# Kernel tuning notes

Measured on AMD Instinct MI355X. Metric: run time of the kernel, lower is better.

## Reference

```python
import jax, jax.numpy as jnp
import numpy as np

DIM, NH, NKV = 1024, 16, 4
HD = DIM // NH  # 64
B, T = 2, 2048


def _rotary_freqs(seq_len, dim):
    inv_freq = 1.0 / (10000.0 ** (jnp.arange(0, dim, 2, dtype=jnp.float32) / dim))
    pos = jnp.arange(seq_len, dtype=jnp.float32)
    return pos[:, None] * inv_freq[None, :]  # [T, dim/2]


def _apply_rotary(x, freqs):
    # x: [B, H, T, HD]; freqs: [T, HD/2]
    x1, x2 = x[..., ::2], x[..., 1::2]
    cos, sin = jnp.cos(freqs), jnp.sin(freqs)
    # NOTE: faithful to source, second half is x1*sin - x2*cos (not +)
    return jnp.concatenate([x1 * cos - x2 * sin, x1 * sin - x2 * cos], axis=-1)


def setup_inputs() -> dict:
    key = jax.random.key(0)
    ks = jax.random.split(key, 5)
    s = 0.02
    return {
        "x": jax.random.normal(ks[0], (B, T, DIM), dtype=jnp.float32),
        "Wq": jax.random.normal(ks[1], (DIM, DIM), dtype=jnp.float32) * s,
        "bq": jnp.zeros((DIM,), jnp.float32),
        "Wk": jax.random.normal(ks[2], (DIM, NKV * HD), dtype=jnp.float32) * s,
        "bk": jnp.zeros((NKV * HD,), jnp.float32),
        "Wv": jax.random.normal(ks[3], (DIM, NKV * HD), dtype=jnp.float32) * s,
        "bv": jnp.zeros((NKV * HD,), jnp.float32),
        "Wo": jax.random.normal(ks[4], (DIM, DIM), dtype=jnp.float32) * s,
        "bo": jnp.zeros((DIM,), jnp.float32),
    }


def reference(x, Wq, bq, Wk, bk, Wv, bv, Wo, bo):
    Bx, Tx, C = x.shape
    q = (x @ Wq + bq).reshape(Bx, Tx, NH, HD).transpose(0, 2, 1, 3)   # [B,NH,T,HD]
    k = (x @ Wk + bk).reshape(Bx, Tx, NKV, HD).transpose(0, 2, 1, 3)  # [B,NKV,T,HD]
    v = (x @ Wv + bv).reshape(Bx, Tx, NKV, HD).transpose(0, 2, 1, 3)

    freqs = _rotary_freqs(Tx, HD)
    q = _apply_rotary(q, freqs)
    k = _apply_rotary(k, freqs)

    rep = NH // NKV
    k = jnp.repeat(k, rep, axis=1)  # [B,NH,T,HD]
    v = jnpp = jnp.repeat(v, rep, axis=1)

    scores = jnp.einsum('bhqd,bhkd->bhqk', q, k) / jnp.sqrt(jnp.float32(HD))
    causal = jnp.tril(jnp.ones((Tx, Tx), dtype=bool))
    scores = jnp.where(causal[None, None], scores, -jnp.inf)
    attn = jax.nn.softmax(scores, axis=-1)
    ctx = jnp.einsum('bhqk,bhkd->bhqd', attn, v)
    out = ctx.transpose(0, 2, 1, 3).reshape(Bx, Tx, C)
    return out @ Wo + bo
```

## Files before the change

### kernel.cpp

```cpp
#include <hip/hip_runtime.h>
#include <math.h>

#define DIM 1024
#define NH 16
#define NKV 4
#define HD 64
#define HALF 32
#define NB 2
#define SEQ 2048
#define KVD 256
#define MTOT 4096
#define QSCALE 0.18033688f
#define MBIAS 8.0f

typedef __bf16 bf16x8 __attribute__((ext_vector_type(8)));
typedef float f32x4 __attribute__((ext_vector_type(4)));
typedef unsigned short u16x8 __attribute__((ext_vector_type(8)));

#define MFMA16(a, b, c) __builtin_amdgcn_mfma_f32_16x16x32_bf16(a, b, c, 0, 0, 0)

__device__ __forceinline__ unsigned short f2bf(float f) {
    unsigned int u = __float_as_uint(f);
    u = (u + 0x7fffu + ((u >> 16) & 1u)) >> 16;
    return (unsigned short)u;
}

__device__ __forceinline__ unsigned cvt_pk(float lo, float hi) {
    unsigned r;
    asm("v_cvt_pk_bf16_f32 %0, %1, %2" : "=v"(r) : "v"(lo), "v"(hi));
    return r;
}

__device__ __forceinline__ void gll16(const unsigned short* g, unsigned short* l) {
    __builtin_amdgcn_global_load_lds((const __attribute__((address_space(1))) void*)g,
                                     (__attribute__((address_space(3))) void*)l, 16, 0, 0);
}

__global__ __launch_bounds__(256) void prep_kernel(
    const float* __restrict__ x,
    const float* __restrict__ Wq, const float* __restrict__ Wk,
    const float* __restrict__ Wv, const float* __restrict__ Wo,
    unsigned short* __restrict__ xb,
    unsigned short* __restrict__ qt, unsigned short* __restrict__ kt,
    unsigned short* __restrict__ vt, unsigned short* __restrict__ ot,
    float* __restrict__ cosb, float* __restrict__ sinb)
{
    __shared__ float tile[64][65];
    const int bx = blockIdx.x;
    const int tid = threadIdx.x;
    if (bx < 256) {
        int idx = bx * 256 + tid;
        int t = idx >> 5, d = idx & 31;
        float e = (float)(2 * d) / (float)HD;
        float invf = 1.0f / powf(10000.0f, e);
        float f = (float)t * invf;
        cosb[idx] = cosf(f);
        sinb[idx] = sinf(f);
    } else if (bx < 2304) {
        int i = ((bx - 256) * 256 + tid) * 8;
        float4 v0 = *(const float4*)&x[i];
        float4 v1 = *(const float4*)&x[i + 4];
        u16x8 o;
        o[0] = f2bf(v0.x); o[1] = f2bf(v0.y); o[2] = f2bf(v0.z); o[3] = f2bf(v0.w);
        o[4] = f2bf(v1.x); o[5] = f2bf(v1.y); o[6] = f2bf(v1.z); o[7] = f2bf(v1.w);
        *(u16x8*)&xb[i] = o;
    } else {
        int idx2 = bx - 2304;
        int z = idx2 >> 8, rem = idx2 & 255, xx = rem & 15, yy = rem >> 4;
        const float* W; unsigned short* Wt; int N;
        switch (z) {
            case 0: W = Wq; Wt = qt; N = DIM; break;
            case 1: W = Wk; Wt = kt; N = KVD; break;
            case 2: W = Wv; Wt = vt; N = KVD; break;
            default: W = Wo; Wt = ot; N = DIM; break;
        }
        const int n0 = xx * 64;
        if (n0 >= N) return;
        const int k0 = yy * 64;
        const int row = tid >> 2, coff = (tid & 3) * 16;
#pragma unroll
        for (int i = 0; i < 4; i++) {
            float4 v = *(const float4*)&W[(size_t)(k0 + row) * N + n0 + coff + i * 4];
            tile[row][coff + i * 4 + 0] = v.x; tile[row][coff + i * 4 + 1] = v.y;
            tile[row][coff + i * 4 + 2] = v.z; tile[row][coff + i * 4 + 3] = v.w;
        }
        __syncthreads();
        u16x8 a, b;
#pragma unroll
        for (int i = 0; i < 8; i++) a[i] = f2bf(tile[coff + i][row]);
#pragma unroll
        for (int i = 0; i < 8; i++) b[i] = f2bf(tile[coff + 8 + i][row]);
        *(u16x8*)&Wt[(size_t)(n0 + row) * DIM + k0 + coff] = a;
        *(u16x8*)&Wt[(size_t)(n0 + row) * DIM + k0 + coff + 8] = b;
    }
}

__global__ __launch_bounds__(256) void qkv_gemm_kernel(
    const unsigned short* __restrict__ xb,
    const unsigned short* __restrict__ wqt, const unsigned short* __restrict__ wkt,
    const unsigned short* __restrict__ wvt,
    const float* __restrict__ bq, const float* __restrict__ bk, const float* __restrict__ bv,
    const float* __restrict__ cosb, const float* __restrict__ sinb,
    unsigned short* __restrict__ qbuf, unsigned short* __restrict__ kbuf,
    unsigned short* __restrict__ vT)
{
    __shared__ unsigned short As[128 * 32];
    __shared__ unsigned short Bs[128 * 32];
    const int tid = threadIdx.x;
    const int lane = tid & 63, w = tid >> 6;
    const int l15 = lane & 15, lg = lane >> 4;
    const int bid = blockIdx.x;
    const int lid = (bid & 7) * 48 + (bid >> 3);
    const int m0 = (lid / 12) * 128;
    const int n0g = (lid % 12) * 128;

    const unsigned short* Wt; const float* bias; int n0, mode;
    if (n0g < DIM)            { Wt = wqt; bias = bq; n0 = n0g; mode = 0; }
    else if (n0g < DIM + KVD) { Wt = wkt; bias = bk; n0 = n0g - DIM; mode = 1; }
    else                      { Wt = wvt; bias = bv; n0 = n0g - DIM - KVD; mode = 2; }

    const int wr = w >> 1, wc = w & 1;

    f32x4 acc[4][4];
#pragma unroll
    for (int i = 0; i < 4; i++)
#pragma unroll
        for (int j = 0; j < 4; j++) acc[i][j] = (f32x4){0.f, 0.f, 0.f, 0.f};

    for (int k0 = 0; k0 < DIM; k0 += 32) {
        __syncthreads();
#pragma unroll
        for (int i = 0; i < 2; i++) {
            int S = i * 256 + w * 64 + lane;
            int r = S >> 2, c8 = (S & 3) * 8;
            gll16(xb + (size_t)(m0 + r) * DIM + k0 + c8, &As[(i * 256 + w * 64) * 8]);
            gll16(Wt + (size_t)(n0 + r) * DIM + k0 + c8, &Bs[(i * 256 + w * 64) * 8]);
        }
        __syncthreads();
        bf16x8 af[4], bfr[4];
#pragma unroll
        for (int r = 0; r < 4; r++)
            af[r] = *(const bf16x8*)&As[(wr * 64 + r * 16 + l15) * 32 + lg * 8];
#pragma unroll
        for (int c = 0; c < 4; c++)
            bfr[c] = *(const bf16x8*)&Bs[(wc * 64 + c * 16 + l15) * 32 + lg * 8];
#pragma unroll
        for (int r = 0; r < 4; r++)
#pragma unroll
            for (int c = 0; c < 4; c++)
                acc[r][c] = MFMA16(af[r], bfr[c], acc[r][c]);
    }

    const int nloc = n0 + wc * 64;
    const bool even = (l15 & 1) == 0;
#pragma unroll
    for (int rt = 0; rt < 4; rt++) {
#pragma unroll
        for (int ct = 0; ct < 4; ct++) {
            const int c = ct * 16 + l15;
            const float bsv = bias[nloc + c];
            if (mode == 2) {
                const int col = nloc + c;
                const int khh = col >> 6, d = col & 63;
                const int bb = m0 >> 11;
                const int t = (m0 & (SEQ - 1)) + wr * 64 + rt * 16 + lg * 4;
                float v0 = acc[rt][ct][0] + bsv;
                float v1 = acc[rt][ct][1] + bsv;
                float v2 = acc[rt][ct][2] + bsv;
                float v3 = acc[rt][ct][3] + bsv;
                unsigned short* dst = vT + ((size_t)(bb * NKV + khh) * 64 + d) * SEQ + t;
                *(uint2*)dst = make_uint2(cvt_pk(v0, v1), cvt_pk(v2, v3));
            } else {
                const int p = c >> 1;
#pragma unroll
                for (int q = 0; q < 4; q++) {
                    const int mrow = m0 + wr * 64 + rt * 16 + lg * 4 + q;
                    float val = acc[rt][ct][q] + bsv;
                    float prt = __shfl_xor(val, 1);
                    const int t = mrow & (SEQ - 1);
                    float cs = cosb[t * HALF + p];
                    float sn = sinb[t * HALF + p];
                    float outv = even ? (val * cs - prt * sn) : (prt * sn - val * cs);
                    int outc = even ? p : (p + 32);
                    if (mode == 0) qbuf[(size_t)mrow * DIM + nloc + outc] = f2bf(outv * QSCALE);
                    else           kbuf[(size_t)mrow * KVD + nloc + outc] = f2bf(outv);
                }
            }
        }
    }
}

__global__ __launch_bounds__(256) void attn_mfma_kernel(
    const unsigned short* __restrict__ qb, const unsigned short* __restrict__ kb,
    const unsigned short* __restrict__ vT, unsigned short* __restrict__ ctx)
{
    __shared__ unsigned short Qs[64 * 64];
    __shared__ unsigned short Ks[2][64 * 64];
    __shared__ unsigned short Vt[2][64 * 64];
    __shared__ unsigned Pw[4][16 * 32];

    const int tid = threadIdx.x;
    const int lane = tid & 63, w = tid >> 6;
    const int l15 = lane & 15, lg = lane >> 4;
    const int xpair = blockIdx.x;
    const int h = blockIdx.y;
    const int b = blockIdx.z;
    const int kh = h >> 2;

    const unsigned short* qg = qb + (size_t)b * SEQ * DIM + (size_t)h * HD;
    const unsigned short* kg = kb + (size_t)b * SEQ * KVD + (size_t)kh * HD;
    const unsigned short* vg = vT + ((size_t)(b * NKV + kh) * HD) * SEQ;

    const int qg_row = w * 16 + l15;
    const int swzd = (l15 & 7) << 3;
    unsigned* PW = &Pw[w][l15 * 32];
    const int pswz = (l15 & 7) << 2;

    const int S1 = w * 64 + lane, r1 = S1 >> 3, d81 = ((S1 & 7) ^ (r1 & 7)) * 8;
    const int S2 = 256 + w * 64 + lane, r2 = S2 >> 3, d82 = ((S2 & 7) ^ (r2 & 7)) * 8;

#pragma unroll 1
    for (int p = 0; p < 2; p++) {
        const int xt = (p == 0) ? xpair : (31 - xpair);
        const int q0 = xt * 64;

        gll16(qg + (size_t)(q0 + r1) * DIM + d81, &Qs[(w * 64) * 8]);
        gll16(qg + (size_t)(q0 + r2) * DIM + d82, &Qs[(256 + w * 64) * 8]);
        gll16(kg + (size_t)r1 * KVD + d81, &Ks[0][(w * 64) * 8]);
        gll16(vg + (size_t)r1 * SEQ + d81, &Vt[0][(w * 64) * 8]);
        gll16(kg + (size_t)r2 * KVD + d82, &Ks[0][(256 + w * 64) * 8]);
        gll16(vg + (size_t)r2 * SEQ + d82, &Vt[0][(256 + w * 64) * 8]);
        __syncthreads();

        bf16x8 bq0 = *(const bf16x8*)&Qs[qg_row * 64 + ((lg * 8) ^ swzd)];
        bf16x8 bq1 = *(const bf16x8*)&Qs[qg_row * 64 + ((32 + lg * 8) ^ swzd)];

        f32x4 o[4];
#pragma unroll
        for (int i = 0; i < 4; i++) o[i] = (f32x4){0.f, 0.f, 0.f, 0.f};
        float lrun = 0.f;

        const int nch = xt + 1;
#pragma unroll 1
        for (int ch = 0; ch < nch; ch++) {
            const int cur = ch & 1;
            if (ch + 1 < nch) {
                const int kv1 = (ch + 1) * 64;
                gll16(kg + (size_t)(kv1 + r1) * KVD + d81, &Ks[cur ^ 1][(w * 64) * 8]);
                gll16(vg + (size_t)r1 * SEQ + kv1 + d81,   &Vt[cur ^ 1][(w * 64) * 8]);
                gll16(kg + (size_t)(kv1 + r2) * KVD + d82, &Ks[cur ^ 1][(256 + w * 64) * 8]);
                gll16(vg + (size_t)r2 * SEQ + kv1 + d82,   &Vt[cur ^ 1][(256 + w * 64) * 8]);
            }

            f32x4 sacc[4];
#pragma unroll
            for (int i = 0; i < 4; i++) sacc[i] = (f32x4){0.f, 0.f, 0.f, 0.f};
            __builtin_amdgcn_s_setprio(1);
#pragma unroll
            for (int ct = 0; ct < 4; ct++) {
                const int kr = ct * 16 + l15;
                bf16x8 ak = *(const bf16x8*)&Ks[cur][kr * 64 + ((lg * 8) ^ swzd)];
                sacc[ct] = MFMA16(ak, bq0, sacc[ct]);
            }
#pragma unroll
            for (int ct = 0; ct < 4; ct++) {
                const int kr = ct * 16 + l15;
                bf16x8 ak = *(const bf16x8*)&Ks[cur][kr * 64 + ((32 + lg * 8) ^ swzd)];
                sacc[ct] = MFMA16(ak, bq1, sacc[ct]);
            }
            __builtin_amdgcn_s_setprio(0);

            const int kv0 = ch * 64;
            if (kv0 == q0) {
#pragma unroll
                for (int ct = 0; ct < 4; ct++)
#pragma unroll
                    for (int r = 0; r < 4; r++)
                        if (ct * 16 + lg * 4 + r > qg_row) sacc[ct][r] = -INFINITY;
            }

            float rs = 0.f;
            unsigned pk0[4], pk1[4];
#pragma unroll
            for (int ct = 0; ct < 4; ct++) {
                float p0 = exp2f(sacc[ct][0] - MBIAS);
                float p1 = exp2f(sacc[ct][1] - MBIAS);
                float p2 = exp2f(sacc[ct][2] - MBIAS);
                float p3 = exp2f(sacc[ct][3] - MBIAS);
                rs += (p0 + p1) + (p2 + p3);
                pk0[ct] = cvt_pk(p0, p1);
                pk1[ct] = cvt_pk(p2, p3);
            }
            rs += __shfl_xor(rs, 16);
            rs += __shfl_xor(rs, 32);
            lrun += rs;

#pragma unroll
            for (int ct = 0; ct < 4; ct++) {
                int wrd = (ct * 8 + lg * 2) ^ pswz;
                *(uint2*)&PW[wrd] = make_uint2(pk0[ct], pk1[ct]);
            }

            __builtin_amdgcn_s_setprio(1);
#pragma unroll
            for (int s = 0; s < 2; s++) {
                int wrd = (s * 16 + lg * 4) ^ pswz;
                bf16x8 ap = *(const bf16x8*)&PW[wrd];
#pragma unroll
                for (int dt = 0; dt < 4; dt++) {
                    const int d = dt * 16 + l15;
                    bf16x8 bv2 = *(const bf16x8*)&Vt[cur][d * 64 + ((s * 32 + lg * 8) ^ ((d & 7) << 3))];
                    o[dt] = MFMA16(ap, bv2, o[dt]);
                }
            }
            __builtin_amdgcn_s_setprio(0);

            __syncthreads();
        }

        float linv = 1.0f / lrun;
        float lb0 = __shfl(linv, lg * 4 + 0);
        float lb1 = __shfl(linv, lg * 4 + 1);
        float lb2 = __shfl(linv, lg * 4 + 2);
        float lb3 = __shfl(linv, lg * 4 + 3);
#pragma unroll
        for (int dt = 0; dt < 4; dt++) {
            const size_t base = (size_t)(b * SEQ + q0 + lg * 4) * DIM + h * HD + dt * 16 + l15;
            ctx[base + (size_t)(w * 16) * DIM]           = f2bf(o[dt][0] * lb0);
            ctx[base + (size_t)(w * 16 + 1) * DIM]       = f2bf(o[dt][1] * lb1);
            ctx[base + (size_t)(w * 16 + 2) * DIM]       = f2bf(o[dt][2] * lb2);
            ctx[base + (size_t)(w * 16 + 3) * DIM]       = f2bf(o[dt][3] * lb3);
        }
    }
}

__global__ __launch_bounds__(256) void outproj_kernel(
    const unsigned short* __restrict__ ctx, const unsigned short* __restrict__ wot,
    const float* __restrict__ bo, float* __restrict__ out)
{
    __shared__ unsigned short As[128 * 32];
    __shared__ unsigned short Bs[128 * 32];
    const int tid = threadIdx.x;
    const int lane = tid & 63, w = tid >> 6;
    const int l15 = lane & 15, lg = lane >> 4;
    const int bid = blockIdx.x;
    const int lid = (bid & 7) * 32 + (bid >> 3);
    const int m0 = (lid >> 3) * 128;
    const int n0 = (lid & 7) * 128;
    const int wr = w >> 1, wc = w & 1;

    f32x4 acc[4][4];
#pragma unroll
    for (int i = 0; i < 4; i++)
#pragma unroll
        for (int j = 0; j < 4; j++) acc[i][j] = (f32x4){0.f, 0.f, 0.f, 0.f};

    for (int k0 = 0; k0 < DIM; k0 += 32) {
        __syncthreads();
#pragma unroll
        for (int i = 0; i < 2; i++) {
            int S = i * 256 + w * 64 + lane;
            int r = S >> 2, c8 = (S & 3) * 8;
            gll16(ctx + (size_t)(m0 + r) * DIM + k0 + c8, &As[(i * 256 + w * 64) * 8]);
            gll16(wot + (size_t)(n0 + r) * DIM + k0 + c8, &Bs[(i * 256 + w * 64) * 8]);
        }
        __syncthreads();
        bf16x8 af[4], bfr[4];
#pragma unroll
        for (int r = 0; r < 4; r++)
            af[r] = *(const bf16x8*)&As[(wr * 64 + r * 16 + l15) * 32 + lg * 8];
#pragma unroll
        for (int c = 0; c < 4; c++)
            bfr[c] = *(const bf16x8*)&Bs[(wc * 64 + c * 16 + l15) * 32 + lg * 8];
#pragma unroll
        for (int r = 0; r < 4; r++)
#pragma unroll
            for (int c = 0; c < 4; c++)
                acc[r][c] = MFMA16(af[r], bfr[c], acc[r][c]);
    }

#pragma unroll
    for (int rt = 0; rt < 4; rt++) {
#pragma unroll
        for (int ct = 0; ct < 4; ct++) {
            const int ncol = n0 + wc * 64 + ct * 16 + l15;
            const float bsv = bo[ncol];
#pragma unroll
            for (int q = 0; q < 4; q++) {
                const int mrow = m0 + wr * 64 + rt * 16 + lg * 4 + q;
                out[(size_t)mrow * DIM + ncol] = acc[rt][ct][q] + bsv;
            }
        }
    }
}

extern "C" void kernel_launch(void* const* d_in, const int* in_sizes, int n_in,
                              void* d_out, int out_size, void* d_ws, size_t ws_size,
                              hipStream_t stream) {
    (void)in_sizes; (void)n_in; (void)out_size; (void)ws_size;
    const float* x  = (const float*)d_in[0];
    const float* Wq = (const float*)d_in[1];
    const float* bq = (const float*)d_in[2];
    const float* Wk = (const float*)d_in[3];
    const float* bk = (const float*)d_in[4];
    const float* Wv = (const float*)d_in[5];
    const float* bv = (const float*)d_in[6];
    const float* Wo = (const float*)d_in[7];
    const float* bo = (const float*)d_in[8];
    float* out = (float*)d_out;
    char* ws = (char*)d_ws;

    unsigned short* xb  = (unsigned short*)(ws);
    unsigned short* qbf = (unsigned short*)(ws + 8388608);
    unsigned short* kbf = (unsigned short*)(ws + 16777216);
    unsigned short* ctx = (unsigned short*)(ws + 20971520);
    unsigned short* wqt = (unsigned short*)(ws + 29360128);
    unsigned short* wkt = (unsigned short*)(ws + 31457280);
    unsigned short* wvt = (unsigned short*)(ws + 31981568);
    unsigned short* wot = (unsigned short*)(ws + 32505856);
    float* cosb = (float*)(ws + 34603008);
    float* sinb = (float*)(ws + 34865152);
    unsigned short* vTb = (unsigned short*)(ws + 35127296);

    hipLaunchKernelGGL(prep_kernel, dim3(3328), dim3(256), 0, stream,
                       x, Wq, Wk, Wv, Wo, xb, wqt, wkt, wvt, wot, cosb, sinb);
    hipLaunchKernelGGL(qkv_gemm_kernel, dim3(384), dim3(256), 0, stream,
                       xb, wqt, wkt, wvt, bq, bk, bv, cosb, sinb, qbf, kbf, vTb);
    hipLaunchKernelGGL(attn_mfma_kernel, dim3(16, NH, NB), dim3(256), 0, stream,
                       qbf, kbf, vTb, ctx);
    hipLaunchKernelGGL(outproj_kernel, dim3(256), dim3(256), 0, stream,
                       ctx, wot, bo, out);
}
```

Baseline: 112.4 us.

## Split paired query tiles into separate blocks and load Q directly to registers

The attention kernel now launches one block per 64-row query tile (32 tiles per head) instead of pairing a short and a long causal tile in one block. Tile order is rotated by the head/batch index to spread the long and short tiles across the grid. Q is read straight from global memory into registers, which drops the Q shared-memory buffer, and the row-sum shuffles are moved out of the inner loop to run once at the end. It also adds an occupancy hint of 4 blocks per CU. The cost is losing the built-in load balancing of paired tiles, so the grid now contains blocks with very uneven amounts of work.

```diff
diff --git a/kernel.cpp b/kernel.cpp
--- a/kernel.cpp
+++ b/kernel.cpp
@@ -190,11 +190,10 @@
     }
 }
 
-__global__ __launch_bounds__(256) void attn_mfma_kernel(
+__global__ __launch_bounds__(256, 4) void attn_mfma_kernel(
     const unsigned short* __restrict__ qb, const unsigned short* __restrict__ kb,
     const unsigned short* __restrict__ vT, unsigned short* __restrict__ ctx)
 {
-    __shared__ unsigned short Qs[64 * 64];
     __shared__ unsigned short Ks[2][64 * 64];
     __shared__ unsigned short Vt[2][64 * 64];
     __shared__ unsigned Pw[4][16 * 32];
@@ -202,12 +201,13 @@
     const int tid = threadIdx.x;
     const int lane = tid & 63, w = tid >> 6;
     const int l15 = lane & 15, lg = lane >> 4;
-    const int xpair = blockIdx.x;
     const int h = blockIdx.y;
     const int b = blockIdx.z;
     const int kh = h >> 2;
-
-    const unsigned short* qg = qb + (size_t)b * SEQ * DIM + (size_t)h * HD;
+    const int g = h + NH * b;
+    const int tile = (blockIdx.x + g) & 31;
+    const int q0 = tile * 64;
+
     const unsigned short* kg = kb + (size_t)b * SEQ * KVD + (size_t)kh * HD;
     const unsigned short* vg = vT + ((size_t)(b * NKV + kh) * HD) * SEQ;
 
@@ -216,121 +216,113 @@
     unsigned* PW = &Pw[w][l15 * 32];
     const int pswz = (l15 & 7) << 2;
 
+    const unsigned short* qptr = qb + ((size_t)(b * SEQ + q0 + qg_row) * DIM + h * HD + lg * 8);
+    bf16x8 bq0 = *(const bf16x8*)qptr;
+    bf16x8 bq1 = *(const bf16x8*)(qptr + 32);
+
     const int S1 = w * 64 + lane, r1 = S1 >> 3, d81 = ((S1 & 7) ^ (r1 & 7)) * 8;
     const int S2 = 256 + w * 64 + lane, r2 = S2 >> 3, d82 = ((S2 & 7) ^ (r2 & 7)) * 8;
 
+    gll16(kg + (size_t)r1 * KVD + d81, &Ks[0][(w * 64) * 8]);
+    gll16(vg + (size_t)r1 * SEQ + d81, &Vt[0][(w * 64) * 8]);
+    gll16(kg + (size_t)r2 * KVD + d82, &Ks[0][(256 + w * 64) * 8]);
+    gll16(vg + (size_t)r2 * SEQ + d82, &Vt[0][(256 + w * 64) * 8]);
+    __syncthreads();
+
+    f32x4 o[4];
+#pragma unroll
+    for (int i = 0; i < 4; i++) o[i] = (f32x4){0.f, 0.f, 0.f, 0.f};
+    float lrun = 0.f;
+
+    const int nch = tile + 1;
 #pragma unroll 1
-    for (int p = 0; p < 2; p++) {
-        const int xt = (p == 0) ? xpair : (31 - xpair);
-        const int q0 = xt * 64;
-
-        gll16(qg + (size_t)(q0 + r1) * DIM + d81, &Qs[(w * 64) * 8]);
-        gll16(qg + (size_t)(q0 + r2) * DIM + d82, &Qs[(256 + w * 64) * 8]);
-        gll16(kg + (size_t)r1 * KVD + d81, &Ks[0][(w * 64) * 8]);
-        gll16(vg + (size_t)r1 * SEQ + d81, &Vt[0][(w * 64) * 8]);
-        gll16(kg + (size_t)r2 * KVD + d82, &Ks[0][(256 + w * 64) * 8]);
-        gll16(vg + (size_t)r2 * SEQ + d82, &Vt[0][(256 + w * 64) * 8]);
-        __syncthreads();
-
-        bf16x8 bq0 = *(const bf16x8*)&Qs[qg_row * 64 + ((lg * 8) ^ swzd)];
-        bf16x8 bq1 = *(const bf16x8*)&Qs[qg_row * 64 + ((32 + lg * 8) ^ swzd)];
-
-        f32x4 o[4];
-#pragma unroll
-        for (int i = 0; i < 4; i++) o[i] = (f32x4){0.f, 0.f, 0.f, 0.f};
-        float lrun = 0.f;
-
-        const int nch = xt + 1;
-#pragma unroll 1
-        for (int ch = 0; ch < nch; ch++) {
-            const int cur = ch & 1;
-            if (ch + 1 < nch) {
-                const int kv1 = (ch + 1) * 64;
-                gll16(kg + (size_t)(kv1 + r1) * KVD + d81, &Ks[cur ^ 1][(w * 64) * 8]);
-                gll16(vg + (size_t)r1 * SEQ + kv1 + d81,   &Vt[cur ^ 1][(w * 64) * 8]);
-                gll16(kg + (size_t)(kv1 + r2) * KVD + d82, &Ks[cur ^ 1][(256 + w * 64) * 8]);
-                gll16(vg + (size_t)r2 * SEQ + kv1 + d82,   &Vt[cur ^ 1][(256 + w * 64) * 8]);
+    for (int ch = 0; ch < nch; ch++) {
+        const int cur = ch & 1;
+        if (ch + 1 < nch) {
+            const int kv1 = (ch + 1) * 64;
+            gll16(kg + (size_t)(kv1 + r1) * KVD + d81, &Ks[cur ^ 1][(w * 64) * 8]);
+            gll16(vg + (size_t)r1 * SEQ + kv1 + d81,   &Vt[cur ^ 1][(w * 64) * 8]);
+            gll16(kg + (size_t)(kv1 + r2) * KVD + d82, &Ks[cur ^ 1][(256 + w * 64) * 8]);
+            gll16(vg + (size_t)r2 * SEQ + kv1 + d82,   &Vt[cur ^ 1][(256 + w * 64) * 8]);
+        }
+
+        f32x4 sacc[4];
+#pragma unroll
+        for (int i = 0; i < 4; i++) sacc[i] = (f32x4){0.f, 0.f, 0.f, 0.f};
+        __builtin_amdgcn_s_setprio(1);
+#pragma unroll
+        for (int ct = 0; ct < 4; ct++) {
+            const int kr = ct * 16 + l15;
+            bf16x8 ak = *(const bf16x8*)&Ks[cur][kr * 64 + ((lg * 8) ^ swzd)];
+            sacc[ct] = MFMA16(ak, bq0, sacc[ct]);
+        }
+#pragma unroll
+        for (int ct = 0; ct < 4; ct++) {
+            const int kr = ct * 16 + l15;
+            bf16x8 ak = *(const bf16x8*)&Ks[cur][kr * 64 + ((32 + lg * 8) ^ swzd)];
+            sacc[ct] = MFMA16(ak, bq1, sacc[ct]);
+        }
+        __builtin_amdgcn_s_setprio(0);
+
+        if (ch == nch - 1) {
+#pragma unroll
+            for (int ct = 0; ct < 4; ct++)
+#pragma unroll
+                for (int r = 0; r < 4; r++)
+                    if (ct * 16 + lg * 4 + r > qg_row) sacc[ct][r] = -INFINITY;
+        }
+
+        float rs = 0.f;
+        unsigned pk0[4], pk1[4];
+#pragma unroll
+        for (int ct = 0; ct < 4; ct++) {
+            float p0 = exp2f(sacc[ct][0] - MBIAS);
+            float p1 = exp2f(sacc[ct][1] - MBIAS);
+            float p2 = exp2f(sacc[ct][2] - MBIAS);
+            float p3 = exp2f(sacc[ct][3] - MBIAS);
+            rs += (p0 + p1) + (p2 + p3);
+            pk0[ct] = cvt_pk(p0, p1);
+            pk1[ct] = cvt_pk(p2, p3);
+        }
+        lrun += rs;
+
+#pragma unroll
+        for (int ct = 0; ct < 4; ct++) {
+            int wrd = (ct * 8 + lg * 2) ^ pswz;
+            *(uint2*)&PW[wrd] = make_uint2(pk0[ct], pk1[ct]);
+        }
+
+        __builtin_amdgcn_s_setprio(1);
+#pragma unroll
+        for (int s = 0; s < 2; s++) {
+            int wrd = (s * 16 + lg * 4) ^ pswz;
+            bf16x8 ap = *(const bf16x8*)&PW[wrd];
+#pragma unroll
+            for (int dt = 0; dt < 4; dt++) {
+                const int d = dt * 16 + l15;
+                bf16x8 bv2 = *(const bf16x8*)&Vt[cur][d * 64 + ((s * 32 + lg * 8) ^ ((d & 7) << 3))];
+                o[dt] = MFMA16(ap, bv2, o[dt]);
             }
-
-            f32x4 sacc[4];
-#pragma unroll
-            for (int i = 0; i < 4; i++) sacc[i] = (f32x4){0.f, 0.f, 0.f, 0.f};
-            __builtin_amdgcn_s_setprio(1);
-#pragma unroll
-            for (int ct = 0; ct < 4; ct++) {
-                const int kr = ct * 16 + l15;
-                bf16x8 ak = *(const bf16x8*)&Ks[cur][kr * 64 + ((lg * 8) ^ swzd)];
-                sacc[ct] = MFMA16(ak, bq0, sacc[ct]);
-            }
-#pragma unroll
-            for (int ct = 0; ct < 4; ct++) {
-                const int kr = ct * 16 + l15;
-                bf16x8 ak = *(const bf16x8*)&Ks[cur][kr * 64 + ((32 + lg * 8) ^ swzd)];
-                sacc[ct] = MFMA16(ak, bq1, sacc[ct]);
-            }
-            __builtin_amdgcn_s_setprio(0);
-
-            const int kv0 = ch * 64;
-            if (kv0 == q0) {
-#pragma unroll
-                for (int ct = 0; ct < 4; ct++)
-#pragma unroll
-                    for (int r = 0; r < 4; r++)
-                        if (ct * 16 + lg * 4 + r > qg_row) sacc[ct][r] = -INFINITY;
-            }
-
-            float rs = 0.f;
-            unsigned pk0[4], pk1[4];
-#pragma unroll
-            for (int ct = 0; ct < 4; ct++) {
-                float p0 = exp2f(sacc[ct][0] - MBIAS);
-                float p1 = exp2f(sacc[ct][1] - MBIAS);
-                float p2 = exp2f(sacc[ct][2] - MBIAS);
-                float p3 = exp2f(sacc[ct][3] - MBIAS);
-                rs += (p0 + p1) + (p2 + p3);
-                pk0[ct] = cvt_pk(p0, p1);
-                pk1[ct] = cvt_pk(p2, p3);
-            }
-            rs += __shfl_xor(rs, 16);
-            rs += __shfl_xor(rs, 32);
-            lrun += rs;
-
-#pragma unroll
-            for (int ct = 0; ct < 4; ct++) {
-                int wrd = (ct * 8 + lg * 2) ^ pswz;
-                *(uint2*)&PW[wrd] = make_uint2(pk0[ct], pk1[ct]);
-            }
-
-            __builtin_amdgcn_s_setprio(1);
-#pragma unroll
-            for (int s = 0; s < 2; s++) {
-                int wrd = (s * 16 + lg * 4) ^ pswz;
-                bf16x8 ap = *(const bf16x8*)&PW[wrd];
-#pragma unroll
-                for (int dt = 0; dt < 4; dt++) {
-                    const int d = dt * 16 + l15;
-                    bf16x8 bv2 = *(const bf16x8*)&Vt[cur][d * 64 + ((s * 32 + lg * 8) ^ ((d & 7) << 3))];
-                    o[dt] = MFMA16(ap, bv2, o[dt]);
-                }
-            }
-            __builtin_amdgcn_s_setprio(0);
-
-            __syncthreads();
-        }
-
-        float linv = 1.0f / lrun;
-        float lb0 = __shfl(linv, lg * 4 + 0);
-        float lb1 = __shfl(linv, lg * 4 + 1);
-        float lb2 = __shfl(linv, lg * 4 + 2);
-        float lb3 = __shfl(linv, lg * 4 + 3);
-#pragma unroll
-        for (int dt = 0; dt < 4; dt++) {
-            const size_t base = (size_t)(b * SEQ + q0 + lg * 4) * DIM + h * HD + dt * 16 + l15;
-            ctx[base + (size_t)(w * 16) * DIM]           = f2bf(o[dt][0] * lb0);
-            ctx[base + (size_t)(w * 16 + 1) * DIM]       = f2bf(o[dt][1] * lb1);
-            ctx[base + (size_t)(w * 16 + 2) * DIM]       = f2bf(o[dt][2] * lb2);
-            ctx[base + (size_t)(w * 16 + 3) * DIM]       = f2bf(o[dt][3] * lb3);
-        }
+        }
+        __builtin_amdgcn_s_setprio(0);
+
+        __syncthreads();
+    }
+
+    lrun += __shfl_xor(lrun, 16);
+    lrun += __shfl_xor(lrun, 32);
+    float linv = 1.0f / lrun;
+    float lb0 = __shfl(linv, lg * 4 + 0);
+    float lb1 = __shfl(linv, lg * 4 + 1);
+    float lb2 = __shfl(linv, lg * 4 + 2);
+    float lb3 = __shfl(linv, lg * 4 + 3);
+#pragma unroll
+    for (int dt = 0; dt < 4; dt++) {
+        const size_t base = (size_t)(b * SEQ + q0 + w * 16 + lg * 4) * DIM + h * HD + dt * 16 + l15;
+        ctx[base]           = f2bf(o[dt][0] * lb0);
+        ctx[base + DIM]     = f2bf(o[dt][1] * lb1);
+        ctx[base + 2 * DIM] = f2bf(o[dt][2] * lb2);
+        ctx[base + 3 * DIM] = f2bf(o[dt][3] * lb3);
     }
 }
 
@@ -426,7 +418,7 @@
                        x, Wq, Wk, Wv, Wo, xb, wqt, wkt, wvt, wot, cosb, sinb);
     hipLaunchKernelGGL(qkv_gemm_kernel, dim3(384), dim3(256), 0, stream,
                        xb, wqt, wkt, wvt, bq, bk, bv, cosb, sinb, qbf, kbf, vTb);
-    hipLaunchKernelGGL(attn_mfma_kernel, dim3(16, NH, NB), dim3(256), 0, stream,
+    hipLaunchKernelGGL(attn_mfma_kernel, dim3(32, NH, NB), dim3(256), 0, stream,
                        qbf, kbf, vTb, ctx);
     hipLaunchKernelGGL(outproj_kernel, dim3(256), dim3(256), 0, stream,
                        ctx, wot, bo, out);
```

Result: no change. 111.0 us (-1.2%).
